# Performance work log

Hardware: AMD Instinct MI355X
Metric: run time of the kernel (lower is better)

The kernel has to match this reference:

```python
import jax, jax.numpy as jnp
import numpy as np

HEAD_NUM = 16
EMBED = 1024

def setup_inputs() -> dict:
    key = jax.random.key(0)
    k1, k2, k3 = jax.random.split(key, 3)
    x = jax.random.normal(k1, (2, 2048, EMBED), dtype=jnp.float32)
    W_qkv = jax.random.normal(k2, (3 * EMBED, EMBED), dtype=jnp.float32) * (EMBED ** -0.5)
    W_out = jax.random.normal(k3, (EMBED, EMBED), dtype=jnp.float32) * (EMBED ** -0.5)
    return {"x": x, "W_qkv": W_qkv, "W_out": W_out}

def reference(x, W_qkv, W_out):
    b, t, E = x.shape
    h = HEAD_NUM
    d = E // h
    dk = (E / h) ** 0.5
    qkv = x @ W_qkv.T  # [b, t, 3E]
    # einops 'b t (d k h) -> k b h t d' with k=3, h=head_num (d outermost in the split)
    qkv = qkv.reshape(b, t, d, 3, h).transpose(3, 0, 4, 1, 2)  # [3, b, h, t, d]
    q, k, v = qkv[0], qkv[1], qkv[2]
    energy = jnp.einsum('bhid,bhjd->bhij', q, k) / dk  # [b, h, t, t]
    attn = jax.nn.softmax(energy, axis=-1)
    out = jnp.einsum('bhij,bhjd->bhid', attn, v)  # [b, h, t, d]
    out = out.transpose(0, 2, 1, 3).reshape(b, t, E)  # 'b h t d -> b t (h d)'
    return out @ W_out.T
```

## Files before the change

### kernel.cpp

```cpp
#include <hip/hip_runtime.h>
#include <hip/hip_bf16.h>


#define HEADS 16
#define EMB   1024
#define HDIM  64
#define BB    2
#define TT    2048
#define QSCALE 0.18033688011112042f

typedef __attribute__((ext_vector_type(8))) short bf16x8;
typedef __attribute__((ext_vector_type(4))) float f32x4;

__device__ __forceinline__ unsigned short f2bf(float f) {
    __hip_bfloat16 h = __float2bfloat16(f);
    return __builtin_bit_cast(unsigned short, h);
}
__device__ __forceinline__ float fexp2(float x) {
#if __has_builtin(__builtin_amdgcn_exp2f)
    return __builtin_amdgcn_exp2f(x);
#else
    return exp2f(x);
#endif
}
__device__ __forceinline__ unsigned pk2t(float x, float y) {
#if __has_builtin(__builtin_amdgcn_perm)
    return __builtin_amdgcn_perm(__builtin_bit_cast(unsigned, y),
                                 __builtin_bit_cast(unsigned, x), 0x07060302u);
#else
    return (__builtin_bit_cast(unsigned, x) >> 16) |
           (__builtin_bit_cast(unsigned, y) & 0xffff0000u);
#endif
}
__device__ __forceinline__ void gload_lds16(const void* g, void* l) {
    __builtin_amdgcn_global_load_lds(
        (const __attribute__((address_space(1))) void*)g,
        (__attribute__((address_space(3))) void*)l, 16, 0, 0);
}
__device__ __forceinline__ int swzi(int row, int blk) {
    return row * 64 + ((blk ^ (row & 7)) << 3);
}

__global__ __launch_bounds__(256)
void conv_bf16(const float* __restrict__ src, unsigned short* __restrict__ dst,
               int n8) {
    int i = blockIdx.x * 256 + threadIdx.x;
    if (i >= n8) return;
    const float4 v0 = ((const float4*)src)[i * 2];
    const float4 v1 = ((const float4*)src)[i * 2 + 1];
    ushort4 a, b;
    a.x = f2bf(v0.x); a.y = f2bf(v0.y); a.z = f2bf(v0.z); a.w = f2bf(v0.w);
    b.x = f2bf(v1.x); b.y = f2bf(v1.y); b.z = f2bf(v1.z); b.w = f2bf(v1.w);
    ((ushort4*)dst)[i * 2]     = a;
    ((ushort4*)dst)[i * 2 + 1] = b;
}

template<int PERM>
__global__ __launch_bounds__(256)
void convw(const float* __restrict__ src, unsigned short* __restrict__ dst) {
    const int np = blockIdx.x;
    const int ns = PERM ? ((np & 63) * 48 + (np >> 10) * 16 + ((np >> 6) & 15))
                        : np;
    const float4 v = ((const float4*)(src + (size_t)ns * 1024))[threadIdx.x];
    ushort4 u;
    u.x = f2bf(v.x); u.y = f2bf(v.y); u.z = f2bf(v.z); u.w = f2bf(v.w);
    ((ushort4*)(dst + (size_t)np * 1024))[threadIdx.x] = u;
}

template<int EPI>
__global__ __launch_bounds__(256)
void gemm_bf16(const unsigned short* __restrict__ Ag,
               const unsigned short* __restrict__ Wg,
               float* __restrict__ Cout,
               unsigned short* __restrict__ QKb,
               unsigned short* __restrict__ Vt) {
    __shared__ __align__(16) unsigned short Ab[128 * 64];
    __shared__ __align__(16) unsigned short Wb[128 * 64];

    const int tid = threadIdx.x, lane = tid & 63, w = tid >> 6;
    const int n0 = blockIdx.x * 128, m0 = blockIdx.y * 128;
    const int wn = (w >> 1) * 64, wm = (w & 1) * 64;
    const int r16 = lane & 15, g = lane >> 4;

    f32x4 acc[4][4];
    #pragma unroll
    for (int i = 0; i < 4; ++i)
        #pragma unroll
        for (int j = 0; j < 4; ++j)
            acc[i][j] = (f32x4){0.f, 0.f, 0.f, 0.f};

    const int srl = lane >> 3;
    const int scb = lane & 7;

    for (int kt = 0; kt < 16; ++kt) {
        __syncthreads();
        const int k0 = kt * 64;
        #pragma unroll
        for (int i = 0; i < 4; ++i) {
            const int row = w * 32 + i * 8 + srl;
            const int cbs = (scb ^ (row & 7)) << 3;
            gload_lds16(Ag + (size_t)(m0 + row) * 1024 + k0 + cbs,
                        Ab + (size_t)(w * 32 + i * 8) * 64);
            gload_lds16(Wg + (size_t)(n0 + row) * 1024 + k0 + cbs,
                        Wb + (size_t)(w * 32 + i * 8) * 64);
        }
        __syncthreads();

        #pragma unroll
        for (int ks = 0; ks < 2; ++ks) {
            bf16x8 xf[4];
            #pragma unroll
            for (int mi = 0; mi < 4; ++mi)
                xf[mi] = *(const bf16x8*)&Ab[swzi(wm + mi * 16 + r16, ks * 4 + g)];
            #pragma unroll
            for (int ni = 0; ni < 4; ++ni) {
                const bf16x8 wf = *(const bf16x8*)&Wb[swzi(wn + ni * 16 + r16, ks * 4 + g)];
                #pragma unroll
                for (int mi = 0; mi < 4; ++mi)
                    acc[ni][mi] = __builtin_amdgcn_mfma_f32_16x16x32_bf16(
                        wf, xf[mi], acc[ni][mi], 0, 0, 0);
            }
        }
    }

    const int gq = g * 4;
    if (EPI == 0) {
        #pragma unroll
        for (int ni = 0; ni < 4; ++ni)
            #pragma unroll
            for (int mi = 0; mi < 4; ++mi) {
                const int m = m0 + wm + mi * 16 + r16;
                *(f32x4*)&Cout[(size_t)m * 1024 + (n0 + wn + ni * 16 + gq)] =
                    acc[ni][mi];
            }
    } else if (n0 < 2048) {
        #pragma unroll
        for (int ni = 0; ni < 4; ++ni) {
            const float qs = (n0 + wn + ni * 16) < 1024 ? QSCALE : 1.0f;
            #pragma unroll
            for (int mi = 0; mi < 4; ++mi) {
                const int m  = m0 + wm + mi * 16 + r16;
                const int np = n0 + wn + ni * 16 + gq;
                ushort4 u;
                u.x = f2bf(acc[ni][mi][0] * qs); u.y = f2bf(acc[ni][mi][1] * qs);
                u.z = f2bf(acc[ni][mi][2] * qs); u.w = f2bf(acc[ni][mi][3] * qs);
                *(ushort4*)&QKb[(size_t)m * 2048 + np] = u;
            }
        }
    } else {
        const int b = m0 >> 11, t0 = m0 & 2047;
        #pragma unroll
        for (int ni = 0; ni < 4; ++ni)
            #pragma unroll
            for (int mi = 0; mi < 4; ++mi) {
                const int t   = t0 + wm + mi * 16 + r16;
                const int nv0 = (n0 - 2048) + wn + ni * 16 + gq;
                #pragma unroll
                for (int j = 0; j < 4; ++j) {
                    const int nv = nv0 + j, h = nv >> 6, d = nv & 63;
                    Vt[(((size_t)(b * HEADS + h)) * HDIM + d) * TT + t] =
                        f2bf(acc[ni][mi][j]);
                }
            }
    }
}

__global__ __launch_bounds__(256)
void attn_mfma(const unsigned short* __restrict__ QKb,
               const unsigned short* __restrict__ Vt,
               unsigned short* __restrict__ AOb) {
    __shared__ __align__(16) unsigned short Ks[2][64 * 64];
    __shared__ __align__(16) unsigned short Vs[2][64 * 64];
    __shared__ __align__(16) unsigned short Pl[4][16 * 64];

    const int tid = threadIdx.x, lane = tid & 63, w = tid >> 6;
    const int qt = blockIdx.x, h = blockIdx.y, b = blockIdx.z;
    const unsigned short* Vsrc = Vt + (size_t)(b * HEADS + h) * HDIM * TT;

    const int r16 = lane & 15, g = lane >> 4;
    const int srl = lane >> 3;
    const int scb = lane & 7;

    bf16x8 qf0, qf1;
    {
        const size_t base =
            ((size_t)(b * TT + qt * 64 + w * 16 + r16)) * 2048 + h * HDIM;
        qf0 = *(const bf16x8*)(QKb + base + g * 8);
        qf1 = *(const bf16x8*)(QKb + base + g * 8 + 32);
    }

    f32x4 o[4];
    #pragma unroll
    for (int c = 0; c < 4; ++c) o[c] = (f32x4){0.f, 0.f, 0.f, 0.f};
    float mrun = -1e30f, lrun = 0.f;

#define STAGEKV(BUF, J0)                                                        \
    do {                                                                        \
        _Pragma("unroll")                                                       \
        for (int i = 0; i < 2; ++i) {                                           \
            const int rl  = w * 16 + i * 8 + srl;                               \
            const int cbs = (scb ^ (rl & 7)) << 3;                              \
            gload_lds16(QKb + (size_t)(b * TT + (J0) + rl) * 2048 + 1024 +      \
                            h * HDIM + cbs,                                     \
                        &Ks[BUF][(w * 16 + i * 8) * 64]);                       \
            gload_lds16(Vsrc + (size_t)rl * TT + (J0) + cbs,                    \
                        &Vs[BUF][(w * 16 + i * 8) * 64]);                       \
        }                                                                       \
    } while (0)

    STAGEKV(0, 0);

    for (int jt = 0; jt < 32; ++jt) {
        const int bb = jt & 1;
        __syncthreads();
        if (jt < 31) STAGEKV(bb ^ 1, (jt + 1) * 64);

        f32x4 st[4];
        #pragma unroll
        for (int kt = 0; kt < 4; ++kt) st[kt] = (f32x4){0.f, 0.f, 0.f, 0.f};
        __builtin_amdgcn_s_setprio(1);
        #pragma unroll
        for (int kt = 0; kt < 4; ++kt) {
            const bf16x8 ka0 = *(const bf16x8*)&Ks[bb][swzi(kt * 16 + r16, g)];
            const bf16x8 ka1 = *(const bf16x8*)&Ks[bb][swzi(kt * 16 + r16, g + 4)];
            st[kt] = __builtin_amdgcn_mfma_f32_16x16x32_bf16(ka0, qf0, st[kt], 0, 0, 0);
            st[kt] = __builtin_amdgcn_mfma_f32_16x16x32_bf16(ka1, qf1, st[kt], 0, 0, 0);
        }
        __builtin_amdgcn_s_setprio(0);

        float pmax = st[0][0];
        #pragma unroll
        for (int kt = 0; kt < 4; ++kt)
            #pragma unroll
            for (int j = 0; j < 4; ++j) pmax = fmaxf(pmax, st[kt][j]);
        pmax = fmaxf(pmax, __shfl_xor(pmax, 16));
        pmax = fmaxf(pmax, __shfl_xor(pmax, 32));

        if (!__all(pmax <= mrun + 11.5f)) {
            const float mnew = fmaxf(mrun, pmax);
            const float corr = fexp2(mrun - mnew);
            float cj[4];
            #pragma unroll
            for (int j = 0; j < 4; ++j) cj[j] = __shfl(corr, g * 4 + j);
            #pragma unroll
            for (int c = 0; c < 4; ++c)
                #pragma unroll
                for (int j = 0; j < 4; ++j) o[c][j] *= cj[j];
            lrun *= corr;
            mrun = mnew;
        }

        float p[4][4];
        float psum = 0.f;
        #pragma unroll
        for (int kt = 0; kt < 4; ++kt)
            #pragma unroll
            for (int j = 0; j < 4; ++j) {
                p[kt][j] = fexp2(st[kt][j] - mrun);
                psum += p[kt][j];
            }
        psum += __shfl_xor(psum, 16);
        psum += __shfl_xor(psum, 32);
        lrun += psum;

        #pragma unroll
        for (int kt = 0; kt < 4; ++kt) {
            const int bw  = kt * 2 + (g >> 1);
            const int idx = r16 * 64 + ((bw ^ (r16 & 7)) << 3) + (g & 1) * 4;
            uint2 uu;
            uu.x = pk2t(p[kt][0], p[kt][1]);
            uu.y = pk2t(p[kt][2], p[kt][3]);
            *(uint2*)&Pl[w][idx] = uu;
        }

        const bf16x8 pa0 = *(const bf16x8*)&Pl[w][swzi(r16, g)];
        const bf16x8 pa1 = *(const bf16x8*)&Pl[w][swzi(r16, g + 4)];
        __builtin_amdgcn_s_setprio(1);
        #pragma unroll
        for (int c = 0; c < 4; ++c) {
            const bf16x8 vb0 = *(const bf16x8*)&Vs[bb][swzi(c * 16 + r16, g)];
            const bf16x8 vb1 = *(const bf16x8*)&Vs[bb][swzi(c * 16 + r16, g + 4)];
            o[c] = __builtin_amdgcn_mfma_f32_16x16x32_bf16(pa0, vb0, o[c], 0, 0, 0);
            o[c] = __builtin_amdgcn_mfma_f32_16x16x32_bf16(pa1, vb1, o[c], 0, 0, 0);
        }
        __builtin_amdgcn_s_setprio(0);
    }
#undef STAGEKV

    const float invl = 1.0f / lrun;
    float ij[4];
    #pragma unroll
    for (int j = 0; j < 4; ++j) ij[j] = __shfl(invl, g * 4 + j);
    #pragma unroll
    for (int c = 0; c < 4; ++c)
        #pragma unroll
        for (int j = 0; j < 4; ++j) {
            const int q = qt * 64 + w * 16 + g * 4 + j;
            AOb[((size_t)(b * TT + q)) * EMB + h * HDIM + c * 16 + r16] =
                f2bf(o[c][j] * ij[j]);
        }
}

extern "C" void kernel_launch(void* const* d_in, const int* in_sizes, int n_in,
                              void* d_out, int out_size, void* d_ws, size_t ws_size,
                              hipStream_t stream) {
    const float* x    = (const float*)d_in[0];
    const float* Wqkv = (const float*)d_in[1];
    const float* Wout = (const float*)d_in[2];
    float* out = (float*)d_out;

    unsigned short* Wqb = (unsigned short*)d_ws;
    unsigned short* Wob = Wqb + 3145728;
    unsigned short* xb  = Wob + 1048576;
    unsigned short* QKb = xb  + 4194304;
    unsigned short* Vt  = QKb + 8388608;
    unsigned short* AOb = Vt  + 4194304;

    conv_bf16<<<2048, 256, 0, stream>>>(x, xb, 524288);
    convw<1><<<3072, 256, 0, stream>>>(Wqkv, Wqb);
    convw<0><<<1024, 256, 0, stream>>>(Wout, Wob);

    gemm_bf16<1><<<dim3(24, 32), 256, 0, stream>>>(xb, Wqb, nullptr, QKb, Vt);

    attn_mfma<<<dim3(32, 16, 2), 256, 0, stream>>>(QKb, Vt, AOb);

    gemm_bf16<0><<<dim3(8, 32), 256, 0, stream>>>(AOb, Wob, out, nullptr, nullptr);
}
```

Measured before the change: 144.3 us.

## Rewrite attention with 32x32 MFMA, register-resident P via permlane swap, fp16 PV

The attention kernel moves from 16x16x32 to 32x32x16 MFMA tiles, with each wave handling 32 query rows and each block 128 queries. This halves the grid and raises data reuse per K/V tile load. The probability tile is no longer round-tripped through LDS; it is packed to fp16 with cvt_pkrtz and rearranged across lanes with v_permlane32_swap, and the PV product uses f16 MFMA with V stored as fp16. Online-softmax rescaling is replaced by a lazy offset that only activates once scores exceed a threshold, which cuts per-tile max and rescale work but risks fp16 overflow or precision loss for other input distributions.

```diff
diff --git a/kernel.cpp b/kernel.cpp
--- a/kernel.cpp
+++ b/kernel.cpp
@@ -9,8 +9,11 @@
 #define TT    2048
 #define QSCALE 0.18033688011112042f
 
-typedef __attribute__((ext_vector_type(8))) short bf16x8;
-typedef __attribute__((ext_vector_type(4))) float f32x4;
+typedef __attribute__((ext_vector_type(8)))  short      bf16x8;
+typedef __attribute__((ext_vector_type(8)))  _Float16   f16x8;
+typedef __attribute__((ext_vector_type(4)))  float      f32x4;
+typedef __attribute__((ext_vector_type(16))) float      f32x16;
+typedef __attribute__((ext_vector_type(4)))  unsigned   u32x4;
 
 __device__ __forceinline__ unsigned short f2bf(float f) {
     __hip_bfloat16 h = __float2bfloat16(f);
@@ -23,14 +26,12 @@
     return exp2f(x);
 #endif
 }
-__device__ __forceinline__ unsigned pk2t(float x, float y) {
-#if __has_builtin(__builtin_amdgcn_perm)
-    return __builtin_amdgcn_perm(__builtin_bit_cast(unsigned, y),
-                                 __builtin_bit_cast(unsigned, x), 0x07060302u);
-#else
-    return (__builtin_bit_cast(unsigned, x) >> 16) |
-           (__builtin_bit_cast(unsigned, y) & 0xffff0000u);
-#endif
+__device__ __forceinline__ unsigned pkrtz(float a, float b) {
+    auto r = __builtin_amdgcn_cvt_pkrtz(a, b);
+    return __builtin_bit_cast(unsigned, r);
+}
+__device__ __forceinline__ unsigned short f2h(float f) {
+    return (unsigned short)(pkrtz(f, 0.f) & 0xffffu);
 }
 __device__ __forceinline__ void gload_lds16(const void* g, void* l) {
     __builtin_amdgcn_global_load_lds(
@@ -39,6 +40,9 @@
 }
 __device__ __forceinline__ int swzi(int row, int blk) {
     return row * 64 + ((blk ^ (row & 7)) << 3);
+}
+__device__ __forceinline__ void pl32swap(unsigned& a, unsigned& b) {
+    asm("v_permlane32_swap_b32 %0, %1" : "+v"(a), "+v"(b));
 }
 
 __global__ __launch_bounds__(256)
@@ -159,53 +163,53 @@
                 for (int j = 0; j < 4; ++j) {
                     const int nv = nv0 + j, h = nv >> 6, d = nv & 63;
                     Vt[(((size_t)(b * HEADS + h)) * HDIM + d) * TT + t] =
-                        f2bf(acc[ni][mi][j]);
+                        f2h(acc[ni][mi][j]);
                 }
             }
     }
 }
 
 __global__ __launch_bounds__(256)
-void attn_mfma(const unsigned short* __restrict__ QKb,
-               const unsigned short* __restrict__ Vt,
-               unsigned short* __restrict__ AOb) {
+void attn32(const unsigned short* __restrict__ QKb,
+            const unsigned short* __restrict__ Vt,
+            unsigned short* __restrict__ AOb) {
     __shared__ __align__(16) unsigned short Ks[2][64 * 64];
     __shared__ __align__(16) unsigned short Vs[2][64 * 64];
-    __shared__ __align__(16) unsigned short Pl[4][16 * 64];
 
     const int tid = threadIdx.x, lane = tid & 63, w = tid >> 6;
+    const int l31 = lane & 31, hi = lane >> 5;
     const int qt = blockIdx.x, h = blockIdx.y, b = blockIdx.z;
     const unsigned short* Vsrc = Vt + (size_t)(b * HEADS + h) * HDIM * TT;
 
-    const int r16 = lane & 15, g = lane >> 4;
+    bf16x8 qf[4];
+    {
+        const unsigned short* qrow =
+            QKb + ((size_t)(b * TT + qt * 128 + w * 32 + l31)) * 2048 + h * HDIM;
+        #pragma unroll
+        for (int dc = 0; dc < 4; ++dc)
+            qf[dc] = *(const bf16x8*)(qrow + dc * 16 + hi * 8);
+    }
+
+    const f32x16 zz = {};
+    f32x16 o0 = {}, o1 = {};
+    float lrun = 0.f, m_off = 0.f;
+    bool offActive = false;
+
     const int srl = lane >> 3;
     const int scb = lane & 7;
 
-    bf16x8 qf0, qf1;
-    {
-        const size_t base =
-            ((size_t)(b * TT + qt * 64 + w * 16 + r16)) * 2048 + h * HDIM;
-        qf0 = *(const bf16x8*)(QKb + base + g * 8);
-        qf1 = *(const bf16x8*)(QKb + base + g * 8 + 32);
-    }
-
-    f32x4 o[4];
-    #pragma unroll
-    for (int c = 0; c < 4; ++c) o[c] = (f32x4){0.f, 0.f, 0.f, 0.f};
-    float mrun = -1e30f, lrun = 0.f;
-
-#define STAGEKV(BUF, J0)                                                        \
-    do {                                                                        \
-        _Pragma("unroll")                                                       \
-        for (int i = 0; i < 2; ++i) {                                           \
-            const int rl  = w * 16 + i * 8 + srl;                               \
-            const int cbs = (scb ^ (rl & 7)) << 3;                              \
-            gload_lds16(QKb + (size_t)(b * TT + (J0) + rl) * 2048 + 1024 +      \
-                            h * HDIM + cbs,                                     \
-                        &Ks[BUF][(w * 16 + i * 8) * 64]);                       \
-            gload_lds16(Vsrc + (size_t)rl * TT + (J0) + cbs,                    \
-                        &Vs[BUF][(w * 16 + i * 8) * 64]);                       \
-        }                                                                       \
+#define STAGEKV(BUF, J0)                                                         \
+    do {                                                                         \
+        _Pragma("unroll")                                                        \
+        for (int i = 0; i < 2; ++i) {                                            \
+            const int rl  = w * 16 + i * 8 + srl;                                \
+            const int cbs = (scb ^ (rl & 7)) << 3;                               \
+            gload_lds16(QKb + (size_t)(b * TT + (J0) + rl) * 2048 + 1024 +       \
+                            h * HDIM + cbs,                                      \
+                        &Ks[BUF][(w * 16 + i * 8) * 64]);                        \
+            gload_lds16(Vsrc + (size_t)rl * TT + (J0) + cbs,                     \
+                        &Vs[BUF][(w * 16 + i * 8) * 64]);                        \
+        }                                                                        \
     } while (0)
 
     STAGEKV(0, 0);
@@ -215,90 +219,102 @@
         __syncthreads();
         if (jt < 31) STAGEKV(bb ^ 1, (jt + 1) * 64);
 
-        f32x4 st[4];
-        #pragma unroll
-        for (int kt = 0; kt < 4; ++kt) st[kt] = (f32x4){0.f, 0.f, 0.f, 0.f};
+        f32x16 st0, st1;
         __builtin_amdgcn_s_setprio(1);
         #pragma unroll
-        for (int kt = 0; kt < 4; ++kt) {
-            const bf16x8 ka0 = *(const bf16x8*)&Ks[bb][swzi(kt * 16 + r16, g)];
-            const bf16x8 ka1 = *(const bf16x8*)&Ks[bb][swzi(kt * 16 + r16, g + 4)];
-            st[kt] = __builtin_amdgcn_mfma_f32_16x16x32_bf16(ka0, qf0, st[kt], 0, 0, 0);
-            st[kt] = __builtin_amdgcn_mfma_f32_16x16x32_bf16(ka1, qf1, st[kt], 0, 0, 0);
+        for (int dc = 0; dc < 4; ++dc) {
+            const bf16x8 ka0 = *(const bf16x8*)&Ks[bb][swzi(l31,      dc * 2 + hi)];
+            const bf16x8 ka1 = *(const bf16x8*)&Ks[bb][swzi(32 + l31, dc * 2 + hi)];
+            if (dc == 0) {
+                st0 = __builtin_amdgcn_mfma_f32_32x32x16_bf16(ka0, qf[0], zz, 0, 0, 0);
+                st1 = __builtin_amdgcn_mfma_f32_32x32x16_bf16(ka1, qf[0], zz, 0, 0, 0);
+            } else {
+                st0 = __builtin_amdgcn_mfma_f32_32x32x16_bf16(ka0, qf[dc], st0, 0, 0, 0);
+                st1 = __builtin_amdgcn_mfma_f32_32x32x16_bf16(ka1, qf[dc], st1, 0, 0, 0);
+            }
         }
         __builtin_amdgcn_s_setprio(0);
 
-        float pmax = st[0][0];
-        #pragma unroll
-        for (int kt = 0; kt < 4; ++kt)
-            #pragma unroll
-            for (int j = 0; j < 4; ++j) pmax = fmaxf(pmax, st[kt][j]);
-        pmax = fmaxf(pmax, __shfl_xor(pmax, 16));
-        pmax = fmaxf(pmax, __shfl_xor(pmax, 32));
-
-        if (!__all(pmax <= mrun + 11.5f)) {
-            const float mnew = fmaxf(mrun, pmax);
-            const float corr = fexp2(mrun - mnew);
-            float cj[4];
-            #pragma unroll
-            for (int j = 0; j < 4; ++j) cj[j] = __shfl(corr, g * 4 + j);
-            #pragma unroll
-            for (int c = 0; c < 4; ++c)
-                #pragma unroll
-                for (int j = 0; j < 4; ++j) o[c][j] *= cj[j];
+        float smax = fmaxf(st0[0], st1[0]);
+        #pragma unroll
+        for (int j = 1; j < 16; ++j)
+            smax = fmaxf(smax, fmaxf(st0[j], st1[j]));
+        if (__builtin_expect(offActive || __any(smax > 14.0f), 0)) {
+            offActive = true;
+            const float rmax = fmaxf(smax, __shfl_xor(smax, 32));
+            const float mnew = fmaxf(m_off, rmax);
+            const float corr = fexp2(m_off - mnew);
             lrun *= corr;
-            mrun = mnew;
-        }
-
-        float p[4][4];
-        float psum = 0.f;
-        #pragma unroll
-        for (int kt = 0; kt < 4; ++kt)
-            #pragma unroll
-            for (int j = 0; j < 4; ++j) {
-                p[kt][j] = fexp2(st[kt][j] - mrun);
-                psum += p[kt][j];
-            }
-        psum += __shfl_xor(psum, 16);
-        psum += __shfl_xor(psum, 32);
-        lrun += psum;
-
-        #pragma unroll
-        for (int kt = 0; kt < 4; ++kt) {
-            const int bw  = kt * 2 + (g >> 1);
-            const int idx = r16 * 64 + ((bw ^ (r16 & 7)) << 3) + (g & 1) * 4;
-            uint2 uu;
-            uu.x = pk2t(p[kt][0], p[kt][1]);
-            uu.y = pk2t(p[kt][2], p[kt][3]);
-            *(uint2*)&Pl[w][idx] = uu;
-        }
-
-        const bf16x8 pa0 = *(const bf16x8*)&Pl[w][swzi(r16, g)];
-        const bf16x8 pa1 = *(const bf16x8*)&Pl[w][swzi(r16, g + 4)];
+            #pragma unroll
+            for (int r = 0; r < 16; ++r) {
+                const int qr = (r & 3) + 8 * (r >> 2) + 4 * hi;
+                const float cr = __shfl(corr, qr);
+                o0[r] *= cr; o1[r] *= cr;
+            }
+            m_off = mnew;
+            #pragma unroll
+            for (int j = 0; j < 16; ++j) { st0[j] -= m_off; st1[j] -= m_off; }
+        }
+
+        float p[32];
+        #pragma unroll
+        for (int j = 0; j < 16; ++j) {
+            p[j]      = fexp2(st0[j]);
+            p[16 + j] = fexp2(st1[j]);
+        }
+        {
+            float t[16];
+            #pragma unroll
+            for (int j = 0; j < 16; ++j) t[j] = p[j] + p[16 + j];
+            #pragma unroll
+            for (int j = 0; j < 8; ++j) t[j] += t[j + 8];
+            #pragma unroll
+            for (int j = 0; j < 4; ++j) t[j] += t[j + 4];
+            lrun += (t[0] + t[1]) + (t[2] + t[3]);
+        }
+
+        unsigned wd[16];
+        #pragma unroll
+        for (int c = 0; c < 4; ++c) {
+            wd[c * 2 + 0]     = pkrtz(p[4 * c + 0],      p[4 * c + 1]);
+            wd[c * 2 + 1]     = pkrtz(p[4 * c + 2],      p[4 * c + 3]);
+            wd[8 + c * 2 + 0] = pkrtz(p[16 + 4 * c + 0], p[16 + 4 * c + 1]);
+            wd[8 + c * 2 + 1] = pkrtz(p[16 + 4 * c + 2], p[16 + 4 * c + 3]);
+        }
+        f16x8 pa[4];
+        #pragma unroll
+        for (int f = 0; f < 4; ++f) {
+            unsigned w0 = wd[f * 4 + 0], w2 = wd[f * 4 + 2];
+            pl32swap(w0, w2);
+            unsigned w1 = wd[f * 4 + 1], w3 = wd[f * 4 + 3];
+            pl32swap(w1, w3);
+            const u32x4 fv = {w0, w1, w2, w3};
+            pa[f] = __builtin_bit_cast(f16x8, fv);
+        }
+
         __builtin_amdgcn_s_setprio(1);
         #pragma unroll
-        for (int c = 0; c < 4; ++c) {
-            const bf16x8 vb0 = *(const bf16x8*)&Vs[bb][swzi(c * 16 + r16, g)];
-            const bf16x8 vb1 = *(const bf16x8*)&Vs[bb][swzi(c * 16 + r16, g + 4)];
-            o[c] = __builtin_amdgcn_mfma_f32_16x16x32_bf16(pa0, vb0, o[c], 0, 0, 0);
-            o[c] = __builtin_amdgcn_mfma_f32_16x16x32_bf16(pa1, vb1, o[c], 0, 0, 0);
+        for (int f = 0; f < 4; ++f) {
+            const f16x8 vb0 = *(const f16x8*)&Vs[bb][swzi(l31,      f * 2 + hi)];
+            const f16x8 vb1 = *(const f16x8*)&Vs[bb][swzi(32 + l31, f * 2 + hi)];
+            o0 = __builtin_amdgcn_mfma_f32_32x32x16_f16(pa[f], vb0, o0, 0, 0, 0);
+            o1 = __builtin_amdgcn_mfma_f32_32x32x16_f16(pa[f], vb1, o1, 0, 0, 0);
         }
         __builtin_amdgcn_s_setprio(0);
     }
 #undef STAGEKV
 
-    const float invl = 1.0f / lrun;
-    float ij[4];
+    lrun += __shfl_xor(lrun, 32);
+    const float inv = 1.0f / lrun;
     #pragma unroll
-    for (int j = 0; j < 4; ++j) ij[j] = __shfl(invl, g * 4 + j);
-    #pragma unroll
-    for (int c = 0; c < 4; ++c)
-        #pragma unroll
-        for (int j = 0; j < 4; ++j) {
-            const int q = qt * 64 + w * 16 + g * 4 + j;
-            AOb[((size_t)(b * TT + q)) * EMB + h * HDIM + c * 16 + r16] =
-                f2bf(o[c][j] * ij[j]);
-        }
+    for (int r = 0; r < 16; ++r) {
+        const int qr = (r & 3) + 8 * (r >> 2) + 4 * hi;
+        const float ir = __shfl(inv, qr);
+        const int q = qt * 128 + w * 32 + qr;
+        unsigned short* dst = AOb + ((size_t)(b * TT + q)) * EMB + h * HDIM + l31;
+        dst[0]  = f2bf(o0[r] * ir);
+        dst[32] = f2bf(o1[r] * ir);
+    }
 }
 
 extern "C" void kernel_launch(void* const* d_in, const int* in_sizes, int n_in,
@@ -322,7 +338,7 @@
 
     gemm_bf16<1><<<dim3(24, 32), 256, 0, stream>>>(xb, Wqb, nullptr, QKb, Vt);
 
-    attn_mfma<<<dim3(32, 16, 2), 256, 0, stream>>>(QKb, Vt, AOb);
+    attn32<<<dim3(16, 16, 2), 256, 0, stream>>>(QKb, Vt, AOb);
 
     gemm_bf16<0><<<dim3(8, 32), 256, 0, stream>>>(AOb, Wob, out, nullptr, nullptr);
 }
```

New measurement: 140.0 us. 3.0% less time.
